# Kernel optimization log

Measured on AMD Instinct MI355X. Metric: run time of the kernel, lower is better.

The kernel has to match this reference:

```python
import jax, jax.numpy as jnp
import numpy as np

EMBED = 256
HEADS = 8
LEVELS = 3
POINTS = 4
MLP = 4
SS = np.array([[100, 100], [50, 50], [25, 25]], np.int32)  # (H, W) per level


def setup_inputs() -> dict:
    key = jax.random.key(0)
    ks = jax.random.split(key, 12)
    B, Q = 2, 128 * 128
    NV = int((SS[:, 0] * SS[:, 1]).sum())
    C = EMBED
    F = C * MLP
    s = 0.02

    def w(k, shape):
        return jax.random.normal(k, shape, jnp.float32) * s

    return dict(
        query=jax.random.normal(ks[0], (B, Q, C), jnp.float32),
        value=jax.random.normal(ks[1], (B, NV, C), jnp.float32),
        query_pos=jax.random.normal(ks[2], (B, Q, C), jnp.float32),
        ref_pts=jax.random.uniform(ks[3], (B, Q, 2), jnp.float32),
        spatial_shapes=SS,
        level_start_index=np.concatenate([[0], np.cumsum(SS[:, 0] * SS[:, 1])[:-1]]).astype(np.int32),
        ln1_g=jnp.ones(C), ln1_b=jnp.zeros(C),
        ln2_g=jnp.ones(C), ln2_b=jnp.zeros(C),
        W_value=w(ks[4], (C, C)), b_value=jnp.zeros(C),
        W_off=w(ks[5], (C, HEADS * LEVELS * POINTS * 2)), b_off=w(ks[6], (HEADS * LEVELS * POINTS * 2,)),
        W_attn=w(ks[7], (C, HEADS * LEVELS * POINTS)), b_attn=jnp.zeros(HEADS * LEVELS * POINTS),
        W_out=w(ks[8], (C, C)), b_out=jnp.zeros(C),
        W_ffn1=w(ks[9], (C, F)), b_ffn1=jnp.zeros(F),
        W_ffn2=w(ks[10], (F, C)), b_ffn2=jnp.zeros(C),
    )


def _layernorm(x, g, b, eps=1e-5):
    m = x.mean(-1, keepdims=True)
    v = ((x - m) ** 2).mean(-1, keepdims=True)
    return (x - m) * jax.lax.rsqrt(v + eps) * g + b


def _bilinear(v, loc, Hl, Wl):
    # v: [BH, Hl*Wl, d]; loc: [BH, Q, P, 2] normalized to [0,1].
    # grid_sample(align_corners=False, padding=zeros): pixel = loc*size - 0.5
    BH, Q, P, _ = loc.shape
    d = v.shape[-1]
    x = loc[..., 0] * Wl - 0.5
    y = loc[..., 1] * Hl - 0.5
    x0f = jnp.floor(x)
    y0f = jnp.floor(y)
    lx = x - x0f
    ly = y - y0f
    x0 = x0f.astype(jnp.int32)
    y0 = y0f.astype(jnp.int32)

    def gather(xi, yi):
        valid = ((xi >= 0) & (xi < Wl) & (yi >= 0) & (yi < Hl)).astype(v.dtype)
        idx = jnp.clip(yi, 0, Hl - 1) * Wl + jnp.clip(xi, 0, Wl - 1)
        g = jnp.take_along_axis(v, idx.reshape(BH, Q * P, 1), axis=1).reshape(BH, Q, P, d)
        return g * valid[..., None]

    w00 = (1 - lx) * (1 - ly)
    w01 = lx * (1 - ly)
    w10 = (1 - lx) * ly
    w11 = lx * ly
    return (gather(x0, y0) * w00[..., None] + gather(x0 + 1, y0) * w01[..., None]
            + gather(x0, y0 + 1) * w10[..., None] + gather(x0 + 1, y0 + 1) * w11[..., None])


def _forward(query, value, query_pos, ref_pts, spatial_shapes,
             ln1_g, ln1_b, ln2_g, ln2_b,
             W_value, b_value, W_off, b_off, W_attn, b_attn, W_out, b_out,
             W_ffn1, b_ffn1, W_ffn2, b_ffn2):
    B, Q, C = query.shape
    Hh, L, P = HEADS, LEVELS, POINTS
    d = C // Hh
    ss = np.asarray(spatial_shapes)
    starts = np.concatenate([[0], np.cumsum(ss[:, 0] * ss[:, 1])])

    # pre-norm + positional embedding (MSDeformAttn adds query_pos)
    qn = _layernorm(query, ln1_g, ln1_b)
    q = qn + query_pos

    # value projection, split heads
    v = (value @ W_value + b_value).reshape(B, -1, Hh, d)

    off = (q @ W_off + b_off).reshape(B, Q, Hh, L, P, 2)
    aw = jax.nn.softmax((q @ W_attn + b_attn).reshape(B, Q, Hh, L * P), axis=-1)
    aw = aw.reshape(B, Q, Hh, L, P)

    # offset normalizer is (W, H) per level
    normalizer = jnp.asarray(ss[:, ::-1].copy(), jnp.float32)
    # bev_value path: ref_pts broadcast over levels
    loc = ref_pts[:, :, None, None, None, :] + off / normalizer[None, None, None, :, None, :]

    out = jnp.zeros((B * Hh, Q, d), query.dtype)
    for l in range(L):
        Hl, Wl = int(ss[l, 0]), int(ss[l, 1])
        v_l = v[:, starts[l]:starts[l + 1]].transpose(0, 2, 1, 3).reshape(B * Hh, Hl * Wl, d)
        loc_l = loc[:, :, :, l].transpose(0, 2, 1, 3, 4).reshape(B * Hh, Q, P, 2)
        sampled = _bilinear(v_l, loc_l, Hl, Wl)  # [BH, Q, P, d]
        w_l = aw[:, :, :, l].transpose(0, 2, 1, 3).reshape(B * Hh, Q, P)
        out = out + (sampled * w_l[..., None]).sum(2)

    out = out.reshape(B, Hh, Q, d).transpose(0, 2, 1, 3).reshape(B, Q, C)
    x = query + (out @ W_out + b_out)

    h = _layernorm(x, ln2_g, ln2_b)
    x = x + (jax.nn.gelu(h @ W_ffn1 + b_ffn1, approximate=False) @ W_ffn2 + b_ffn2)
    return x


def reference(query, value, query_pos, ref_pts, spatial_shapes, level_start_index,
              ln1_g, ln1_b, ln2_g, ln2_b,
              W_value, b_value, W_off, b_off, W_attn, b_attn, W_out, b_out,
              W_ffn1, b_ffn1, W_ffn2, b_ffn2):
    return _forward(query, value, query_pos, ref_pts, spatial_shapes,
                    ln1_g, ln1_b, ln2_g, ln2_b,
                    W_value, b_value, W_off, b_off, W_attn, b_attn, W_out, b_out,
                    W_ffn1, b_ffn1, W_ffn2, b_ffn2)
```

## Files before the change

### kernel.cpp

```cpp
#include <hip/hip_runtime.h>
#include <hip/hip_bf16.h>

#define BQ      2
#define QLEN    16384
#define CDIM    256
#define HEADS   8
#define LEV     3
#define PTS     4
#define DHEAD   32
#define NVTOT   13125
#define FDIM    1024
#define NTOK    (BQ*QLEN)
#define MROWS_V (BQ*NVTOT)
#define NPROJ   288

typedef __attribute__((ext_vector_type(8))) short short8;
typedef __attribute__((ext_vector_type(4))) float floatx4;
typedef unsigned long long u64;

typedef const __attribute__((address_space(1))) unsigned int gu32;
typedef __attribute__((address_space(3))) unsigned int lu32;

__device__ __forceinline__ int imin(int a, int b){ return a<b?a:b; }
__device__ __forceinline__ int imax(int a, int b){ return a>b?a:b; }

__device__ __forceinline__ float bf2f(unsigned short u){ return __uint_as_float((unsigned)u << 16); }
__device__ __forceinline__ unsigned short f2bf(float f)
{
    __hip_bfloat16 h = __float2bfloat16(f);
    return *(unsigned short*)&h;
}
__device__ __forceinline__ u64 pack4(float4 v)
{
    return (u64)f2bf(v.x) | ((u64)f2bf(v.y) << 16)
         | ((u64)f2bf(v.z) << 32) | ((u64)f2bf(v.w) << 48);
}
__device__ __forceinline__ float4 unpack4(u64 c)
{
    float4 v;
    v.x = bf2f((unsigned short)(c));
    v.y = bf2f((unsigned short)(c >> 16));
    v.z = bf2f((unsigned short)(c >> 32));
    v.w = bf2f((unsigned short)(c >> 48));
    return v;
}

__device__ __forceinline__ float gelu_f(float x)
{
    float u2 = x * x;
    float a  = x * fmaf(0.0713548163f, u2, 1.5957691216f);
    float e  = __expf(a);
    float r  = __builtin_amdgcn_rcpf(e + 1.0f);
    return fmaf(-x, r, x);
}

__device__ __forceinline__ void ln_core(float4 v, const float* __restrict__ pos, int tok,
                                        const float* __restrict__ g, const float* __restrict__ b,
                                        int lane, __hip_bfloat16* __restrict__ out)
{
    float s = v.x + v.y + v.z + v.w;
    #pragma unroll
    for (int o = 32; o > 0; o >>= 1) s += __shfl_down(s, o);
    s = __shfl(s, 0);
    float mean = s * (1.0f / 256.0f);
    float4 c; c.x = v.x - mean; c.y = v.y - mean; c.z = v.z - mean; c.w = v.w - mean;
    float q2 = c.x*c.x + c.y*c.y + c.z*c.z + c.w*c.w;
    #pragma unroll
    for (int o = 32; o > 0; o >>= 1) q2 += __shfl_down(q2, o);
    q2 = __shfl(q2, 0);
    float rstd = rsqrtf(q2 * (1.0f / 256.0f) + 1e-5f);
    float4 gg = ((const float4*)g)[lane];
    float4 bb = ((const float4*)b)[lane];
    float4 o4;
    o4.x = c.x * rstd * gg.x + bb.x;
    o4.y = c.y * rstd * gg.y + bb.y;
    o4.z = c.z * rstd * gg.z + bb.z;
    o4.w = c.w * rstd * gg.w + bb.w;
    if (pos) {
        float4 p = ((const float4*)(pos + (size_t)tok * CDIM))[lane];
        o4.x += p.x; o4.y += p.y; o4.z += p.z; o4.w += p.w;
    }
    *(u64*)(out + (size_t)tok * CDIM + lane * 4) = pack4(o4);
}

#define WT_BLOCKS  2946
#define CVT_BLOCKS 6563
#define LN_BLOCKS  8192

__global__ __launch_bounds__(256)
void prep_k(const float* __restrict__ Wv,  const float* __restrict__ Woff,
            const float* __restrict__ Wat, const float* __restrict__ Wout,
            const float* __restrict__ W1,  const float* __restrict__ W2,
            const float* __restrict__ boff, const float* __restrict__ bat,
            const float* __restrict__ value, const float* __restrict__ query,
            const float* __restrict__ qpos,  const float* __restrict__ ln1g,
            const float* __restrict__ ln1b,
            __hip_bfloat16* __restrict__ o_v,  __hip_bfloat16* __restrict__ o_c,
            __hip_bfloat16* __restrict__ o_out,
            __hip_bfloat16* __restrict__ o_1,  __hip_bfloat16* __restrict__ o_2,
            float* __restrict__ o_bc,
            __hip_bfloat16* __restrict__ vbf,  __hip_bfloat16* __restrict__ qbf)
{
    int bx = blockIdx.x;
    if (bx < WT_BLOCKS) {
        int gid = bx * 256 + threadIdx.x;
        if (gid < 65536) {
            int idx = gid, n = idx >> 8, k = idx & 255;
            o_v[idx] = __float2bfloat16(Wv[(size_t)k * 256 + n]);
        } else if (gid < 163840) {
            int idx = gid - 65536, n = idx >> 8, k = idx & 255;
            float v = 0.0f;
            if (n < 192)       v = Woff[(size_t)k * 192 + n];
            else if (n < 288)  v = Wat[(size_t)k * 96 + (n - 192)];
            o_c[idx] = __float2bfloat16(v);
        } else if (gid < 229376) {
            int idx = gid - 163840, n = idx >> 8, k = idx & 255;
            o_out[idx] = __float2bfloat16(Wout[(size_t)k * 256 + n]);
        } else if (gid < 491520) {
            int idx = gid - 229376, n = idx >> 8, k = idx & 255;
            o_1[idx] = __float2bfloat16(W1[(size_t)k * 1024 + n]);
        } else if (gid < 753664) {
            int idx = gid - 491520, n = idx >> 10, k = idx & 1023;
            o_2[idx] = __float2bfloat16(W2[(size_t)k * 256 + n]);
        } else if (gid < 753952) {
            int idx = gid - 753664;
            o_bc[idx] = (idx < 192) ? boff[idx] : bat[idx - 192];
        }
    } else if (bx < WT_BLOCKS + CVT_BLOCKS) {
        int i = (bx - WT_BLOCKS) * 256 + threadIdx.x;
        if (i < MROWS_V * CDIM / 4) {
            float4 v = ((const float4*)value)[i];
            *(u64*)(vbf + (size_t)i * 4) = pack4(v);
        }
    } else {
        int tok  = (bx - WT_BLOCKS - CVT_BLOCKS) * 4 + (threadIdx.x >> 6);
        int lane = threadIdx.x & 63;
        float4 v = ((const float4*)(query + (size_t)tok * CDIM))[lane];
        ln_core(v, qpos, tok, ln1g, ln1b, lane, qbf);
    }
}

__global__ __launch_bounds__(256)
void ln2_k(const __hip_bfloat16* __restrict__ x, const float* __restrict__ g,
           const float* __restrict__ b, __hip_bfloat16* __restrict__ out)
{
    int tok  = blockIdx.x * 4 + (threadIdx.x >> 6);
    int lane = threadIdx.x & 63;
    float4 v = unpack4(((const u64*)(x + (size_t)tok * CDIM))[lane]);
    ln_core(v, nullptr, tok, g, b, lane, out);
}

enum { EP_PLAIN_BF16 = 0, EP_GELU_BF16 = 1, EP_RES_F2BF = 2, EP_RES_BF2F = 3 };

__global__ __launch_bounds__(256)
void mm_k(const __hip_bfloat16* __restrict__ A, const __hip_bfloat16* __restrict__ Bt,
          const float* __restrict__ bias, const void* __restrict__ res,
          void* __restrict__ Cout, int M, int N, int K, int mode)
{
    __shared__ float4 smem4[2048];
    __hip_bfloat16* Ws = (__hip_bfloat16*)smem4;
    __hip_bfloat16* Ts = (__hip_bfloat16*)smem4 + 128*64;
    u64* st = (u64*)smem4;
    int t = threadIdx.x;
    int lane = t & 63;
    int wave = t >> 6;
    int wm = wave >> 1, wn = wave & 1;
    int lm = lane & 15, lk = lane >> 4;
    int m0 = blockIdx.x * 128;
    int n0 = blockIdx.y * 128;

    floatx4 acc[4][4];
    #pragma unroll
    for (int i = 0; i < 4; i++)
        #pragma unroll
        for (int j = 0; j < 4; j++) acc[i][j] = (floatx4)0.0f;

    for (int kt = 0; kt < K; kt += 64) {
        #pragma unroll
        for (int i = 0; i < 4; i++) {
            int cc  = i * 256 + t;
            int row = cc >> 3;
            int c   = cc & 7;
            int kc  = c ^ (row & 7);
            int ra  = m0 + row; if (ra >= M) ra = M - 1;
            const __hip_bfloat16* gw = Bt + (size_t)(n0 + row) * K + kt + kc * 8;
            const __hip_bfloat16* gt = A  + (size_t)ra * K + kt + kc * 8;
            __builtin_amdgcn_global_load_lds((gu32*)gw, (lu32*)(Ws + cc * 8), 16, 0, 0);
            __builtin_amdgcn_global_load_lds((gu32*)gt, (lu32*)(Ts + cc * 8), 16, 0, 0);
        }
        __syncthreads();
        #pragma unroll
        for (int ks = 0; ks < 2; ks++) {
            short8 wf[4], tf[4];
            #pragma unroll
            for (int i = 0; i < 4; i++) {
                int rw = wn * 64 + i * 16 + lm;
                int cw = (ks * 4 + lk) ^ (rw & 7);
                wf[i] = *(const short8*)(Ws + (rw * 8 + cw) * 8);
                int rt = wm * 64 + i * 16 + lm;
                int ct = (ks * 4 + lk) ^ (rt & 7);
                tf[i] = *(const short8*)(Ts + (rt * 8 + ct) * 8);
            }
            #pragma unroll
            for (int i = 0; i < 4; i++)
                #pragma unroll
                for (int j = 0; j < 4; j++)
                    acc[i][j] = __builtin_amdgcn_mfma_f32_16x16x32_bf16(wf[i], tf[j], acc[i][j], 0, 0, 0);
        }
        __syncthreads();
    }

    #pragma unroll
    for (int i = 0; i < 4; i++) {
        int chan = n0 + wn * 64 + i * 16 + lk * 4;
        float4 b4 = make_float4(0.f, 0.f, 0.f, 0.f);
        if (chan < N) b4 = *(const float4*)(bias + chan);
        int c4 = wn * 16 + i * 4 + lk;
        #pragma unroll
        for (int j = 0; j < 4; j++) {
            int tl = wm * 64 + j * 16 + lm;
            float4 v;
            v.x = acc[i][j][0] + b4.x;
            v.y = acc[i][j][1] + b4.y;
            v.z = acc[i][j][2] + b4.z;
            v.w = acc[i][j][3] + b4.w;
            st[tl * 32 + (c4 ^ (tl & 31))] = pack4(v);
        }
    }
    __syncthreads();

    int rel = (t & 31) * 4;
    int c4r = t & 31;
    #pragma unroll
    for (int it = 0; it < 16; it++) {
        int tl   = it * 8 + (t >> 5);
        int tok  = m0 + tl;
        int chan = n0 + rel;
        if (tok >= M || chan >= N) continue;
        u64 chunk = st[tl * 32 + (c4r ^ (tl & 31))];
        if (mode == EP_PLAIN_BF16) {
            *(u64*)((__hip_bfloat16*)Cout + (size_t)tok * N + chan) = chunk;
        } else if (mode == EP_GELU_BF16) {
            float4 v = unpack4(chunk);
            v.x = gelu_f(v.x); v.y = gelu_f(v.y); v.z = gelu_f(v.z); v.w = gelu_f(v.w);
            *(u64*)((__hip_bfloat16*)Cout + (size_t)tok * N + chan) = pack4(v);
        } else if (mode == EP_RES_F2BF) {
            float4 v = unpack4(chunk);
            float4 rr = *(const float4*)((const float*)res + (size_t)tok * N + chan);
            v.x += rr.x; v.y += rr.y; v.z += rr.z; v.w += rr.w;
            *(u64*)((__hip_bfloat16*)Cout + (size_t)tok * N + chan) = pack4(v);
        } else {
            float4 v = unpack4(chunk);
            float4 rr = unpack4(*(const u64*)((const __hip_bfloat16*)res + (size_t)tok * N + chan));
            v.x += rr.x; v.y += rr.y; v.z += rr.z; v.w += rr.w;
            *(float4*)((float*)Cout + (size_t)tok * N + chan) = v;
        }
    }
}

__global__ __launch_bounds__(512, 2)
void ffn_k(const __hip_bfloat16* __restrict__ h,
           const __hip_bfloat16* __restrict__ W1t,
           const float* __restrict__ b1,
           const __hip_bfloat16* __restrict__ W2t,
           const float* __restrict__ b2,
           const __hip_bfloat16* __restrict__ xres,
           float* __restrict__ out)
{
    extern __shared__ char smem_dyn[];
    __hip_bfloat16* As = (__hip_bfloat16*)smem_dyn;

    int t    = threadIdx.x;
    int lane = t & 63;
    int wave = t >> 6;
    int wm   = wave >> 2;
    int wn   = wave & 3;
    int lm   = lane & 15, lk = lane >> 4;
    int m0   = blockIdx.x * 128;

    #pragma unroll
    for (int i = 0; i < 8; i++) {
        int cc  = i * 512 + t;
        int kt  = cc >> 10;
        int rem = cc & 1023;
        int row = rem >> 3;
        int c   = rem & 7;
        int kc  = c ^ (row & 7);
        const __hip_bfloat16* src = h + (size_t)(m0 + row) * 256 + kt * 64 + kc * 8;
        __builtin_amdgcn_global_load_lds((gu32*)src, (lu32*)(As + cc * 8), 16, 0, 0);
    }

    floatx4 acc2[4][4];
    #pragma unroll
    for (int i = 0; i < 4; i++)
        #pragma unroll
        for (int j = 0; j < 4; j++) acc2[i][j] = (floatx4)0.0f;

    __syncthreads();

    #pragma unroll 1
    for (int fc = 0; fc < 8; fc++) {
        int f0 = fc * 128;
        __hip_bfloat16* gs = (__hip_bfloat16*)(smem_dyn + 65536 + (fc & 1) * 32768);

        floatx4 acc1[2][4];
        #pragma unroll
        for (int i = 0; i < 2; i++)
            #pragma unroll
            for (int j = 0; j < 4; j++) acc1[i][j] = (floatx4)0.0f;

        short8 w1f[8][2];
        #pragma unroll
        for (int kt = 0; kt < 4; kt++)
            #pragma unroll
            for (int ks = 0; ks < 2; ks++)
                #pragma unroll
                for (int i = 0; i < 2; i++)
                    w1f[kt * 2 + ks][i] = *(const short8*)(W1t
                        + (size_t)(f0 + wn * 32 + i * 16 + lm) * 256
                        + kt * 64 + ks * 32 + lk * 8);

        #pragma unroll
        for (int kt = 0; kt < 4; kt++) {
            #pragma unroll
            for (int ks = 0; ks < 2; ks++) {
                short8 tf[4];
                #pragma unroll
                for (int j = 0; j < 4; j++) {
                    int rt = wm * 64 + j * 16 + lm;
                    int ct = (ks * 4 + lk) ^ (rt & 7);
                    tf[j] = *(const short8*)(As + (kt * 1024 + rt * 8 + ct) * 8);
                }
                #pragma unroll
                for (int i = 0; i < 2; i++)
                    #pragma unroll
                    for (int j = 0; j < 4; j++)
                        acc1[i][j] = __builtin_amdgcn_mfma_f32_16x16x32_bf16(
                            w1f[kt * 2 + ks][i], tf[j], acc1[i][j], 0, 0, 0);
            }
        }

        #pragma unroll
        for (int i = 0; i < 2; i++) {
            float4 bb = *(const float4*)(b1 + f0 + wn * 32 + i * 16 + lk * 4);
            int c = wn * 4 + i * 2 + (lk >> 1);
            #pragma unroll
            for (int j = 0; j < 4; j++) {
                int tok = wm * 64 + j * 16 + lm;
                float4 v;
                v.x = gelu_f(acc1[i][j][0] + bb.x);
                v.y = gelu_f(acc1[i][j][1] + bb.y);
                v.z = gelu_f(acc1[i][j][2] + bb.z);
                v.w = gelu_f(acc1[i][j][3] + bb.w);
                int sc = c ^ (tok & 7);
                *(u64*)((char*)gs + tok * 256 + sc * 16 + (lk & 1) * 8) = pack4(v);
            }
        }

        short8 w2f[4][4];
        #pragma unroll
        for (int ks2 = 0; ks2 < 4; ks2++)
            #pragma unroll
            for (int i2 = 0; i2 < 4; i2++)
                w2f[ks2][i2] = *(const short8*)(W2t
                    + (size_t)(wn * 64 + i2 * 16 + lm) * 1024
                    + f0 + ks2 * 32 + lk * 8);

        __syncthreads();

        #pragma unroll
        for (int ks2 = 0; ks2 < 4; ks2++) {
            short8 tf2[4];
            #pragma unroll
            for (int j = 0; j < 4; j++) {
                int tok = wm * 64 + j * 16 + lm;
                int sc = (ks2 * 4 + lk) ^ (tok & 7);
                tf2[j] = *(const short8*)((char*)gs + tok * 256 + sc * 16);
            }
            #pragma unroll
            for (int i2 = 0; i2 < 4; i2++)
                #pragma unroll
                for (int j = 0; j < 4; j++)
                    acc2[i2][j] = __builtin_amdgcn_mfma_f32_16x16x32_bf16(
                        w2f[ks2][i2], tf2[j], acc2[i2][j], 0, 0, 0);
        }
    }

    #pragma unroll
    for (int i2 = 0; i2 < 4; i2++) {
        int c0 = wn * 64 + i2 * 16 + lk * 4;
        float4 bb = *(const float4*)(b2 + c0);
        #pragma unroll
        for (int j = 0; j < 4; j++) {
            int tok = m0 + wm * 64 + j * 16 + lm;
            float4 r = unpack4(*(const u64*)(xres + (size_t)tok * 256 + c0));
            float4 v;
            v.x = acc2[i2][j][0] + bb.x + r.x;
            v.y = acc2[i2][j][1] + bb.y + r.y;
            v.z = acc2[i2][j][2] + bb.z + r.z;
            v.w = acc2[i2][j][3] + bb.w + r.w;
            *(float4*)(out + (size_t)tok * 256 + c0) = v;
        }
    }
}

__global__ __launch_bounds__(256, 6)
void sample_k(const __hip_bfloat16* __restrict__ v, const __hip_bfloat16* __restrict__ cbuf,
              const float* __restrict__ ref, __hip_bfloat16* __restrict__ out)
{
    __shared__ int4   metaIdx[4 * 104];
    __shared__ float4 metaW[4 * 104];

    int wid  = threadIdx.x >> 6;
    int lane = threadIdx.x & 63;
    int t    = blockIdx.x * 4 + wid;
    int b    = t >> 14;
    float rx = ref[(size_t)t * 2 + 0];
    float ry = ref[(size_t)t * 2 + 1];
    const __hip_bfloat16* crow = cbuf + (size_t)t * NPROJ;

    #pragma unroll
    for (int rnd = 0; rnd < 2; rnd++) {
        int slot = rnd * 64 + lane;
        int h = slot >> 4, p = slot & 15;
        int pc = imin(p, 11);
        unsigned upk = *(const unsigned*)(crow + h * 24 + pc * 2);
        float ox = bf2f((unsigned short)upk);
        float oy = bf2f((unsigned short)(upk >> 16));
        float logit = bf2f(*(const unsigned short*)(crow + 192 + h * 12 + pc));
        float mx = logit;
        #pragma unroll
        for (int o = 8; o > 0; o >>= 1) mx = fmaxf(mx, __shfl_xor(mx, o, 16));
        float e = (p < 12) ? __expf(logit - mx) : 0.0f;
        float ssum = e;
        #pragma unroll
        for (int o = 8; o > 0; o >>= 1) ssum += __shfl_xor(ssum, o, 16);
        float aw = e * __builtin_amdgcn_rcpf(ssum);

        if (p < 12) {
            int l = p >> 2;
            float fS = (l == 0) ? 100.0f : ((l == 1) ? 50.0f : 25.0f);
            int   Wl = (l == 0) ? 100 : ((l == 1) ? 50 : 25);
            int   st = (l == 0) ? 0 : ((l == 1) ? 10000 : 12500);
            float x = fmaf(rx, fS, ox) - 0.5f;
            float y = fmaf(ry, fS, oy) - 0.5f;
            float x0f = floorf(x), y0f = floorf(y);
            float fx = x - x0f, fy = y - y0f;
            int x0 = (int)x0f, y0 = (int)y0f;
            int x1 = x0 + 1,  y1 = y0 + 1;
            int cx0 = imin(imax(x0, 0), Wl - 1), cx1 = imin(imax(x1, 0), Wl - 1);
            int cy0 = imin(imax(y0, 0), Wl - 1), cy1 = imin(imax(y1, 0), Wl - 1);
            float vx0 = (x0 >= 0 && x0 < Wl) ? 1.0f : 0.0f;
            float vx1 = (x1 >= 0 && x1 < Wl) ? 1.0f : 0.0f;
            float vy0 = (y0 >= 0 && y0 < Wl) ? 1.0f : 0.0f;
            float vy1 = (y1 >= 0 && y1 < Wl) ? 1.0f : 0.0f;
            int s = wid * 104 + h * 13 + p;
            metaIdx[s] = make_int4((st + cy0 * Wl + cx0) << 9, (st + cy0 * Wl + cx1) << 9,
                                   (st + cy1 * Wl + cx0) << 9, (st + cy1 * Wl + cx1) << 9);
            metaW[s] = make_float4((1.0f - fx) * (1.0f - fy) * aw * vx0 * vy0,
                                   fx * (1.0f - fy) * aw * vx1 * vy0,
                                   (1.0f - fx) * fy * aw * vx0 * vy1,
                                   fx * fy * aw * vx1 * vy1);
        }
    }
    __syncthreads();

    int h  = lane >> 3;
    int bs = __builtin_amdgcn_readfirstlane(b);
    const char* vb = (const char*)(v + (size_t)bs * NVTOT * CDIM);
    int hoff = lane * 8;
    int sB   = wid * 104 + h * 13;
    float4 acc = {0.0f, 0.0f, 0.0f, 0.0f};

    int4   miA = metaIdx[sB + 0];
    float4 mwA = metaW[sB + 0];
    u64 a0 = *(const u64*)(vb + (unsigned)(miA.x + hoff));
    u64 a1 = *(const u64*)(vb + (unsigned)(miA.y + hoff));
    u64 a2 = *(const u64*)(vb + (unsigned)(miA.z + hoff));
    u64 a3 = *(const u64*)(vb + (unsigned)(miA.w + hoff));
    int4   miB = metaIdx[sB + 1];
    float4 mwB = metaW[sB + 1];
    u64 b0 = *(const u64*)(vb + (unsigned)(miB.x + hoff));
    u64 b1 = *(const u64*)(vb + (unsigned)(miB.y + hoff));
    u64 b2 = *(const u64*)(vb + (unsigned)(miB.z + hoff));
    u64 b3 = *(const u64*)(vb + (unsigned)(miB.w + hoff));

    #pragma unroll
    for (int p = 0; p < 12; p++) {
        int pn = (p < 10) ? (p + 2) : 11;
        int4   miN = metaIdx[sB + pn];
        float4 mwN = metaW[sB + pn];
        u64 n0 = *(const u64*)(vb + (unsigned)(miN.x + hoff));
        u64 n1 = *(const u64*)(vb + (unsigned)(miN.y + hoff));
        u64 n2 = *(const u64*)(vb + (unsigned)(miN.z + hoff));
        u64 n3 = *(const u64*)(vb + (unsigned)(miN.w + hoff));

        {
            unsigned d0 = (unsigned)a0, d1 = (unsigned)(a0 >> 32);
            acc.x = fmaf(mwA.x, __uint_as_float(d0 << 16), acc.x);
            acc.y = fmaf(mwA.x, __uint_as_float(d0 & 0xffff0000u), acc.y);
            acc.z = fmaf(mwA.x, __uint_as_float(d1 << 16), acc.z);
            acc.w = fmaf(mwA.x, __uint_as_float(d1 & 0xffff0000u), acc.w);
        }
        {
            unsigned d0 = (unsigned)a1, d1 = (unsigned)(a1 >> 32);
            acc.x = fmaf(mwA.y, __uint_as_float(d0 << 16), acc.x);
            acc.y = fmaf(mwA.y, __uint_as_float(d0 & 0xffff0000u), acc.y);
            acc.z = fmaf(mwA.y, __uint_as_float(d1 << 16), acc.z);
            acc.w = fmaf(mwA.y, __uint_as_float(d1 & 0xffff0000u), acc.w);
        }
        {
            unsigned d0 = (unsigned)a2, d1 = (unsigned)(a2 >> 32);
            acc.x = fmaf(mwA.z, __uint_as_float(d0 << 16), acc.x);
            acc.y = fmaf(mwA.z, __uint_as_float(d0 & 0xffff0000u), acc.y);
            acc.z = fmaf(mwA.z, __uint_as_float(d1 << 16), acc.z);
            acc.w = fmaf(mwA.z, __uint_as_float(d1 & 0xffff0000u), acc.w);
        }
        {
            unsigned d0 = (unsigned)a3, d1 = (unsigned)(a3 >> 32);
            acc.x = fmaf(mwA.w, __uint_as_float(d0 << 16), acc.x);
            acc.y = fmaf(mwA.w, __uint_as_float(d0 & 0xffff0000u), acc.y);
            acc.z = fmaf(mwA.w, __uint_as_float(d1 << 16), acc.z);
            acc.w = fmaf(mwA.w, __uint_as_float(d1 & 0xffff0000u), acc.w);
        }

        a0 = b0; a1 = b1; a2 = b2; a3 = b3; mwA = mwB;
        b0 = n0; b1 = n1; b2 = n2; b3 = n3; mwB = mwN;
    }
    *(u64*)(out + (size_t)t * CDIM + lane * 4) = pack4(acc);
}

extern "C" void kernel_launch(void* const* d_in, const int* in_sizes, int n_in,
                              void* d_out, int out_size, void* d_ws, size_t ws_size,
                              hipStream_t stream)
{
    const float* query = (const float*)d_in[0];
    const float* value = (const float*)d_in[1];
    const float* qpos  = (const float*)d_in[2];
    const float* ref   = (const float*)d_in[3];
    const float* ln1g  = (const float*)d_in[6];
    const float* ln1b  = (const float*)d_in[7];
    const float* ln2g  = (const float*)d_in[8];
    const float* ln2b  = (const float*)d_in[9];
    const float* Wv    = (const float*)d_in[10];
    const float* bv    = (const float*)d_in[11];
    const float* Woff  = (const float*)d_in[12];
    const float* boff  = (const float*)d_in[13];
    const float* Wat   = (const float*)d_in[14];
    const float* bat   = (const float*)d_in[15];
    const float* Wout  = (const float*)d_in[16];
    const float* bout  = (const float*)d_in[17];
    const float* W1    = (const float*)d_in[18];
    const float* b1    = (const float*)d_in[19];
    const float* W2    = (const float*)d_in[20];
    const float* b2    = (const float*)d_in[21];
    float* out = (float*)d_out;
    char*  ws  = (char*)d_ws;

    static bool attr_set = false;
    if (!attr_set) {
        hipFuncSetAttribute((const void*)ffn_k,
                            hipFuncAttributeMaxDynamicSharedMemorySize, 131072);
        attr_set = true;
    }

    const size_t MB = 1024 * 1024;
    __hip_bfloat16* Wvt   = (__hip_bfloat16*)(ws + 0);
    __hip_bfloat16* Wct   = (__hip_bfloat16*)(ws + 131072);
    __hip_bfloat16* Woutt = (__hip_bfloat16*)(ws + 327680);
    __hip_bfloat16* W1t   = (__hip_bfloat16*)(ws + 458752);
    __hip_bfloat16* W2t   = (__hip_bfloat16*)(ws + 983040);
    float*          bcomb = (float*)(ws + 1507328);
    __hip_bfloat16* qbf   = (__hip_bfloat16*)(ws + 2  * MB);
    __hip_bfloat16* aoutb = (__hip_bfloat16*)(ws + 19 * MB);
    __hip_bfloat16* vbf   = (__hip_bfloat16*)(ws + 36 * MB);
    __hip_bfloat16* vbuf  = (__hip_bfloat16*)(ws + 50 * MB);
    __hip_bfloat16* xbf   = (__hip_bfloat16*)(ws + 64 * MB);
    __hip_bfloat16* cbuf  = (__hip_bfloat16*)(ws + 81 * MB);
    __hip_bfloat16* hbf   = qbf;

    prep_k<<<WT_BLOCKS + CVT_BLOCKS + LN_BLOCKS, 256, 0, stream>>>(
        Wv, Woff, Wat, Wout, W1, W2, boff, bat, value, query, qpos, ln1g, ln1b,
        Wvt, Wct, Woutt, W1t, W2t, bcomb, vbf, qbf);
    mm_k<<<dim3((MROWS_V + 127) / 128, 2), 256, 0, stream>>>(
        vbf, Wvt, bv, nullptr, vbuf, MROWS_V, 256, 256, EP_PLAIN_BF16);
    mm_k<<<dim3(NTOK / 128, 3), 256, 0, stream>>>(
        qbf, Wct, bcomb, nullptr, cbuf, NTOK, NPROJ, 256, EP_PLAIN_BF16);
    sample_k<<<NTOK / 4, 256, 0, stream>>>(vbuf, cbuf, ref, aoutb);
    mm_k<<<dim3(NTOK / 128, 2), 256, 0, stream>>>(
        aoutb, Woutt, bout, query, xbf, NTOK, 256, 256, EP_RES_F2BF);
    ln2_k<<<NTOK / 4, 256, 0, stream>>>(xbf, ln2g, ln2b, hbf);
    ffn_k<<<NTOK / 128, 512, 131072, stream>>>(hbf, W1t, b1, W2t, b2, xbf, out);
}
```

Before: 352.8 us.

## Pre-swizzle FFN weights into fragment order and prefetch next W1 chunk

The weight-prep kernel now writes W1 and W2 in the exact per-lane MFMA fragment order, so each lane's 16-byte load in the FFN kernel is fully coalesced across the wave instead of strided by rows. The FFN kernel also loads the next chunk's W1 fragments during the current chunk (software prefetch into registers) to hide global latency behind the second GEMM. This adds 16 more short8 registers per thread, which at launch bounds 512x2 could cause spills or limit occupancy.

```diff
diff --git a/kernel.cpp b/kernel.cpp
--- a/kernel.cpp
+++ b/kernel.cpp
@@ -117,11 +117,29 @@
             int idx = gid - 163840, n = idx >> 8, k = idx & 255;
             o_out[idx] = __float2bfloat16(Wout[(size_t)k * 256 + n]);
         } else if (gid < 491520) {
-            int idx = gid - 229376, n = idx >> 8, k = idx & 255;
-            o_1[idx] = __float2bfloat16(W1[(size_t)k * 1024 + n]);
+            int idx  = gid - 229376;
+            int e    = idx & 7;
+            int c    = idx >> 3;
+            int lane = c & 63, lm = lane & 15, lk = lane >> 4;
+            int r    = (c >> 6) & 15;
+            int wn   = (c >> 10) & 3;
+            int fc   = c >> 12;
+            int i    = r & 1, ks = (r >> 1) & 1, kt = r >> 2;
+            int row  = fc * 128 + wn * 32 + i * 16 + lm;
+            int col  = kt * 64 + ks * 32 + lk * 8 + e;
+            o_1[idx] = __float2bfloat16(W1[(size_t)col * 1024 + row]);
         } else if (gid < 753664) {
-            int idx = gid - 491520, n = idx >> 10, k = idx & 1023;
-            o_2[idx] = __float2bfloat16(W2[(size_t)k * 256 + n]);
+            int idx  = gid - 491520;
+            int e    = idx & 7;
+            int c    = idx >> 3;
+            int lane = c & 63, lm = lane & 15, lk = lane >> 4;
+            int r    = (c >> 6) & 15;
+            int wn   = (c >> 10) & 3;
+            int fc   = c >> 12;
+            int i2   = r & 3, ks2 = r >> 2;
+            int row  = wn * 64 + i2 * 16 + lm;
+            int col  = fc * 128 + ks2 * 32 + lk * 8 + e;
+            o_2[idx] = __float2bfloat16(W2[(size_t)col * 256 + row]);
         } else if (gid < 753952) {
             int idx = gid - 753664;
             o_bc[idx] = (idx < 192) ? boff[idx] : bat[idx - 192];
@@ -260,9 +278,9 @@
 
 __global__ __launch_bounds__(512, 2)
 void ffn_k(const __hip_bfloat16* __restrict__ h,
-           const __hip_bfloat16* __restrict__ W1t,
+           const __hip_bfloat16* __restrict__ W1p,
            const float* __restrict__ b1,
-           const __hip_bfloat16* __restrict__ W2t,
+           const __hip_bfloat16* __restrict__ W2p,
            const float* __restrict__ b2,
            const __hip_bfloat16* __restrict__ xres,
            float* __restrict__ out)
@@ -277,6 +295,10 @@
     int wn   = wave & 3;
     int lm   = lane & 15, lk = lane >> 4;
     int m0   = blockIdx.x * 128;
+
+    const short8* W1v = (const short8*)W1p;
+    const short8* W2v = (const short8*)W2p;
+    int wb = wn * 1024 + lane;
 
     #pragma unroll
     for (int i = 0; i < 8; i++) {
@@ -296,6 +318,10 @@
         #pragma unroll
         for (int j = 0; j < 4; j++) acc2[i][j] = (floatx4)0.0f;
 
+    short8 w1c[16];
+    #pragma unroll
+    for (int r = 0; r < 16; r++) w1c[r] = W1v[wb + r * 64];
+
     __syncthreads();
 
     #pragma unroll 1
@@ -308,17 +334,6 @@
         for (int i = 0; i < 2; i++)
             #pragma unroll
             for (int j = 0; j < 4; j++) acc1[i][j] = (floatx4)0.0f;
-
-        short8 w1f[8][2];
-        #pragma unroll
-        for (int kt = 0; kt < 4; kt++)
-            #pragma unroll
-            for (int ks = 0; ks < 2; ks++)
-                #pragma unroll
-                for (int i = 0; i < 2; i++)
-                    w1f[kt * 2 + ks][i] = *(const short8*)(W1t
-                        + (size_t)(f0 + wn * 32 + i * 16 + lm) * 256
-                        + kt * 64 + ks * 32 + lk * 8);
 
         #pragma unroll
         for (int kt = 0; kt < 4; kt++) {
@@ -336,7 +351,7 @@
                     #pragma unroll
                     for (int j = 0; j < 4; j++)
                         acc1[i][j] = __builtin_amdgcn_mfma_f32_16x16x32_bf16(
-                            w1f[kt * 2 + ks][i], tf[j], acc1[i][j], 0, 0, 0);
+                            w1c[kt * 4 + ks * 2 + i], tf[j], acc1[i][j], 0, 0, 0);
             }
         }
 
@@ -357,14 +372,14 @@
             }
         }
 
-        short8 w2f[4][4];
-        #pragma unroll
-        for (int ks2 = 0; ks2 < 4; ks2++)
-            #pragma unroll
-            for (int i2 = 0; i2 < 4; i2++)
-                w2f[ks2][i2] = *(const short8*)(W2t
-                    + (size_t)(wn * 64 + i2 * 16 + lm) * 1024
-                    + f0 + ks2 * 32 + lk * 8);
+        short8 w2f[16];
+        #pragma unroll
+        for (int r = 0; r < 16; r++) w2f[r] = W2v[fc * 4096 + wb + r * 64];
+
+        short8 w1n[16];
+        int fcn = (fc < 7) ? fc + 1 : 7;
+        #pragma unroll
+        for (int r = 0; r < 16; r++) w1n[r] = W1v[fcn * 4096 + wb + r * 64];
 
         __syncthreads();
 
@@ -382,8 +397,11 @@
                 #pragma unroll
                 for (int j = 0; j < 4; j++)
                     acc2[i2][j] = __builtin_amdgcn_mfma_f32_16x16x32_bf16(
-                        w2f[ks2][i2], tf2[j], acc2[i2][j], 0, 0, 0);
-        }
+                        w2f[ks2 * 4 + i2], tf2[j], acc2[i2][j], 0, 0, 0);
+        }
+
+        #pragma unroll
+        for (int r = 0; r < 16; r++) w1c[r] = w1n[r];
     }
 
     #pragma unroll
```

Result: faster. 329.7 us (-6.5%).
